# Kernel optimization log

Hardware: AMD Instinct MI355X
Metric: run time of the kernel (lower is better)

Reference implementation:

```python
import jax, jax.numpy as jnp
import numpy as np

B = 1024          # batch of subject-object pairs
D_IN_HALF = 2048  # sbj/obj feature width; cat -> input_len = 4096
D_OUT = 1024      # output_len (embedding / label-vec width)
N_LABELS = 128    # number of relation labels in codebook


def setup_inputs() -> dict:
    key = jax.random.key(0)
    ks = jax.random.split(key, 7)
    s = 0.02  # small init scale for weights
    return {
        "sbj_vec": jax.random.normal(ks[0], (B, D_IN_HALF), jnp.float32),
        "obj_vec": jax.random.normal(ks[1], (B, D_IN_HALF), jnp.float32),
        "W1": jax.random.normal(ks[2], (2 * D_IN_HALF, D_OUT), jnp.float32) * s,
        "b1": jax.random.normal(ks[3], (D_OUT,), jnp.float32) * s,
        "W2": jax.random.normal(ks[4], (D_OUT, D_OUT), jnp.float32) * s,
        "b2": jax.random.normal(ks[5], (D_OUT,), jnp.float32) * s,
        "label_vecs": jax.random.normal(ks[6], (N_LABELS, D_OUT), jnp.float32),
    }


def reference(sbj_vec, obj_vec, W1, b1, W2, b2, label_vecs):
    # Sequential(ReLU, Dropout(eval=identity), Linear) applied twice.
    x = jnp.concatenate([sbj_vec, obj_vec], axis=1)          # [B, 2*D_IN_HALF]
    hidden = jax.nn.relu(x) @ W1 + b1                        # [B, D_OUT]
    emb = jax.nn.relu(hidden) @ W2 + b2                      # [B, D_OUT]
    # order_sim vs every label vector, fully batched (replaces per-sample loop):
    # sim[b, l] = -|| relu(label_vecs[l] - emb[b]) ||_2
    diff = jax.nn.relu(label_vecs[None, :, :] - emb[:, None, :])  # [B, L, D_OUT]
    scores = -jnp.sqrt(jnp.sum(diff * diff, axis=2))              # [B, L]
    return scores
```

## Files before the change

kernel.cpp:

```cpp
#include <hip/hip_runtime.h>
#include <math.h>

constexpr int Bn = 1024, DH = 2048, K1 = 4096, DO = 1024, NL = 128;
constexpr int MN = Bn * DO;

typedef __bf16 bf16x8 __attribute__((ext_vector_type(8)));
typedef short  s16x8  __attribute__((ext_vector_type(8)));
typedef float  f32x4  __attribute__((ext_vector_type(4)));

__device__ __forceinline__ unsigned short f2bf(float f) {
  union { float f; unsigned u; } v; v.f = f;
  unsigned r = v.u + 0x7FFFu + ((v.u >> 16) & 1u);
  return (unsigned short)(r >> 16);
}
__device__ __forceinline__ float bf2f(unsigned h) {
  union { unsigned u; float f; } v; v.u = h << 16; return v.f;
}

__global__ __launch_bounds__(256)
void prep(const float* __restrict__ sbj, const float* __restrict__ obj,
          const float* __restrict__ W1, const float* __restrict__ W2,
          unsigned short* __restrict__ Abf,
          unsigned short* __restrict__ W1t, unsigned short* __restrict__ W2t) {
  const int tid = threadIdx.x;
  if (blockIdx.x < 2048) {
    const int t = blockIdx.x * 256 + tid;
    const int m = t >> 9;
    const int k = (t & 511) << 3;
    const float* src = (k < DH) ? sbj + (size_t)m * DH + k
                                : obj + (size_t)m * DH + (k - DH);
    const float4 a = ((const float4*)src)[0];
    const float4 b = ((const float4*)src)[1];
    uint4 o;
    o.x = (unsigned)f2bf(fmaxf(a.x, 0.f)) | ((unsigned)f2bf(fmaxf(a.y, 0.f)) << 16);
    o.y = (unsigned)f2bf(fmaxf(a.z, 0.f)) | ((unsigned)f2bf(fmaxf(a.w, 0.f)) << 16);
    o.z = (unsigned)f2bf(fmaxf(b.x, 0.f)) | ((unsigned)f2bf(fmaxf(b.y, 0.f)) << 16);
    o.w = (unsigned)f2bf(fmaxf(b.z, 0.f)) | ((unsigned)f2bf(fmaxf(b.w, 0.f)) << 16);
    *(uint4*)&Abf[(size_t)m * K1 + k] = o;
    return;
  }
  __shared__ float tl[64][65];
  const int tb = blockIdx.x - 2048;
  int by = tb >> 4;
  const int c0 = (tb & 15) * 64;
  const float* in; unsigned short* out; int R;
  if (by < 64) { in = W1; out = W1t; R = K1; }
  else         { in = W2; out = W2t; R = DO; by -= 64; }
  const int r0 = by * 64;
  {
    const int rr = tid >> 4, cc = (tid & 15) * 4;
    #pragma unroll
    for (int i = 0; i < 4; ++i) {
      const float4 v = *(const float4*)&in[(size_t)(r0 + rr + i * 16) * DO + c0 + cc];
      tl[rr + i * 16][cc + 0] = v.x; tl[rr + i * 16][cc + 1] = v.y;
      tl[rr + i * 16][cc + 2] = v.z; tl[rr + i * 16][cc + 3] = v.w;
    }
  }
  __syncthreads();
  {
    const int r4 = (tid & 15) * 4;
    #pragma unroll
    for (int i = 0; i < 4; ++i) {
      const int cr = i * 16 + (tid >> 4);
      uint2 o;
      o.x = (unsigned)f2bf(tl[r4 + 0][cr]) | ((unsigned)f2bf(tl[r4 + 1][cr]) << 16);
      o.y = (unsigned)f2bf(tl[r4 + 2][cr]) | ((unsigned)f2bf(tl[r4 + 3][cr]) << 16);
      *(uint2*)&out[(size_t)(c0 + cr) * R + r0 + r4] = o;
    }
  }
}

template <int KSLICE>
__global__ __launch_bounds__(256, 2)
void mfma_gemm(const unsigned short* __restrict__ A,
               const unsigned short* __restrict__ Bt,
               unsigned short* __restrict__ P, int K) {
  __shared__ __align__(16) unsigned short smem[2 * 128 * 64];
  unsigned short* LA = smem;
  unsigned short* LB = smem + 128 * 64;

  const int tid = threadIdx.x;
  const int w = tid >> 6, l = tid & 63;
  const int bid = blockIdx.x;
  const int z = bid & 7, t = bid >> 3;
  const int m0 = (t >> 3) * 128, n0 = (t & 7) * 128;
  const int kb = z * KSLICE;

  f32x4 acc[4][4] = {};

  constexpr int NIT = KSLICE / 64;
  for (int it = 0; it < NIT; ++it) {
    const int k0 = kb + it * 64;
    #pragma unroll
    for (int i = 0; i < 4; ++i) {
      const int c = i * 256 + tid, row = c >> 3, kc = c & 7;
      const int kcg = kc ^ (row & 7);
      __builtin_amdgcn_global_load_lds(
          (const __attribute__((address_space(1))) unsigned int*)(A + (size_t)(m0 + row) * K + k0 + kcg * 8),
          (__attribute__((address_space(3))) unsigned int*)&LA[c * 8], 16, 0, 0);
    }
    #pragma unroll
    for (int i = 0; i < 4; ++i) {
      const int c = i * 256 + tid, row = c >> 3, kc = c & 7;
      const int kcg = kc ^ (row & 7);
      __builtin_amdgcn_global_load_lds(
          (const __attribute__((address_space(1))) unsigned int*)(Bt + (size_t)(n0 + row) * K + k0 + kcg * 8),
          (__attribute__((address_space(3))) unsigned int*)&LB[c * 8], 16, 0, 0);
    }
    __syncthreads();

    #pragma unroll
    for (int s = 0; s < 2; ++s) {
      const int kcq = s * 4 + (l >> 4);
      bf16x8 af[4], bfr[4];
      #pragma unroll
      for (int i = 0; i < 4; ++i) {
        const int r = (w >> 1) * 64 + i * 16 + (l & 15);
        const int kca = kcq ^ (r & 7);
        af[i] = __builtin_bit_cast(bf16x8, *(const s16x8*)&LA[(r * 8 + kca) * 8]);
      }
      #pragma unroll
      for (int j = 0; j < 4; ++j) {
        const int rr = (w & 1) * 64 + j * 16 + (l & 15);
        const int kcb = kcq ^ (rr & 7);
        bfr[j] = __builtin_bit_cast(bf16x8, *(const s16x8*)&LB[(rr * 8 + kcb) * 8]);
      }
      #pragma unroll
      for (int i = 0; i < 4; ++i)
        #pragma unroll
        for (int j = 0; j < 4; ++j)
          acc[i][j] = __builtin_amdgcn_mfma_f32_16x16x32_bf16(af[i], bfr[j], acc[i][j], 0, 0, 0);
    }
    __syncthreads();
  }

  unsigned short* Pz = P + (size_t)z * MN;
  #pragma unroll
  for (int i = 0; i < 4; ++i) {
    #pragma unroll
    for (int r = 0; r < 4; ++r) {
      const int m = m0 + (w >> 1) * 64 + i * 16 + (l >> 4) * 4 + r;
      #pragma unroll
      for (int j = 0; j < 4; ++j) {
        const int n = n0 + (w & 1) * 64 + j * 16 + (l & 15);
        Pz[(size_t)m * DO + n] = f2bf(acc[i][j][r]);
      }
    }
  }
}

__global__ __launch_bounds__(256)
void combine1(const unsigned short* __restrict__ P, const float* __restrict__ bias,
              unsigned short* __restrict__ out) {
  const int row = blockIdx.x, t = threadIdx.x;
  const size_t base = (size_t)row * DO + t * 4;
  float s0 = 0.f, s1 = 0.f, s2 = 0.f, s3 = 0.f;
  #pragma unroll
  for (int c = 0; c < 8; ++c) {
    const uint2 wv = *(const uint2*)&P[(size_t)c * MN + base];
    s0 += bf2f(wv.x & 0xFFFFu); s1 += bf2f(wv.x >> 16);
    s2 += bf2f(wv.y & 0xFFFFu); s3 += bf2f(wv.y >> 16);
  }
  const f32x4 bb = *(const f32x4*)&bias[t * 4];
  s0 = fmaxf(s0 + bb[0], 0.f); s1 = fmaxf(s1 + bb[1], 0.f);
  s2 = fmaxf(s2 + bb[2], 0.f); s3 = fmaxf(s3 + bb[3], 0.f);
  uint2 o;
  o.x = (unsigned)f2bf(s0) | ((unsigned)f2bf(s1) << 16);
  o.y = (unsigned)f2bf(s2) | ((unsigned)f2bf(s3) << 16);
  *(uint2*)&out[base] = o;
}

__global__ __launch_bounds__(256, 4)
void gemm2_full(const unsigned short* __restrict__ A,
                const unsigned short* __restrict__ Bt,
                const float* __restrict__ b2, float* __restrict__ E) {
  __shared__ __align__(16) unsigned short smem[2 * 64 * 128];
  unsigned short* LA = smem;
  unsigned short* LB = smem + 64 * 128;

  const int tid = threadIdx.x;
  const int w = tid >> 6, l = tid & 63;
  const int bid = blockIdx.x;
  const int m0 = (bid >> 4) * 64, n0 = (bid & 15) * 64;

  f32x4 acc[4][4] = {};

  for (int it = 0; it < 8; ++it) {
    const int k0 = it * 128;
    #pragma unroll
    for (int i = 0; i < 4; ++i) {
      const int c = i * 256 + tid, m = c >> 4, kc = c & 15;
      const int kcg = (kc & 8) | ((kc & 7) ^ (m & 7));
      __builtin_amdgcn_global_load_lds(
          (const __attribute__((address_space(1))) unsigned int*)(A + (size_t)(m0 + m) * DO + k0 + kcg * 8),
          (__attribute__((address_space(3))) unsigned int*)&LA[c * 8], 16, 0, 0);
    }
    #pragma unroll
    for (int i = 0; i < 4; ++i) {
      const int c = i * 256 + tid, n = c >> 4, kc = c & 15;
      const int kcg = (kc & 8) | ((kc & 7) ^ (n & 7));
      __builtin_amdgcn_global_load_lds(
          (const __attribute__((address_space(1))) unsigned int*)(Bt + (size_t)(n0 + n) * DO + k0 + kcg * 8),
          (__attribute__((address_space(3))) unsigned int*)&LB[c * 8], 16, 0, 0);
    }
    __syncthreads();

    const int kcq = w * 4 + (l >> 4);
    bf16x8 af[4], bfr[4];
    #pragma unroll
    for (int i = 0; i < 4; ++i) {
      const int r = i * 16 + (l & 15);
      const int kca = (kcq & 8) | ((kcq & 7) ^ (r & 7));
      af[i]  = __builtin_bit_cast(bf16x8, *(const s16x8*)&LA[(r * 16 + kca) * 8]);
      bfr[i] = __builtin_bit_cast(bf16x8, *(const s16x8*)&LB[(r * 16 + kca) * 8]);
    }
    #pragma unroll
    for (int i = 0; i < 4; ++i)
      #pragma unroll
      for (int j = 0; j < 4; ++j)
        acc[i][j] = __builtin_amdgcn_mfma_f32_16x16x32_bf16(af[i], bfr[j], acc[i][j], 0, 0, 0);
    __syncthreads();
  }

  float* red = (float*)smem;
  if (w >= 2) {
    #pragma unroll
    for (int i = 0; i < 4; ++i)
      #pragma unroll
      for (int j = 0; j < 4; ++j)
        *(f32x4*)&red[(w - 2) * 4096 + ((i * 4 + j) * 64 + l) * 4] = acc[i][j];
  }
  __syncthreads();
  if (w < 2) {
    #pragma unroll
    for (int i = 0; i < 4; ++i)
      #pragma unroll
      for (int j = 0; j < 4; ++j)
        acc[i][j] += *(const f32x4*)&red[w * 4096 + ((i * 4 + j) * 64 + l) * 4];
  }
  __syncthreads();
  if (w == 1) {
    #pragma unroll
    for (int i = 0; i < 2; ++i)
      #pragma unroll
      for (int j = 0; j < 4; ++j)
        *(f32x4*)&red[((i * 4 + j) * 64 + l) * 4] = acc[i][j];
  } else if (w == 0) {
    #pragma unroll
    for (int i = 0; i < 2; ++i)
      #pragma unroll
      for (int j = 0; j < 4; ++j)
        *(f32x4*)&red[2048 + ((i * 4 + j) * 64 + l) * 4] = acc[i + 2][j];
  }
  __syncthreads();
  if (w >= 2) return;

  if (w == 0) {
    #pragma unroll
    for (int i = 0; i < 2; ++i) {
      #pragma unroll
      for (int j = 0; j < 4; ++j)
        acc[i][j] += *(const f32x4*)&red[((i * 4 + j) * 64 + l) * 4];
      #pragma unroll
      for (int r = 0; r < 4; ++r) {
        const int m = m0 + i * 16 + (l >> 4) * 4 + r;
        #pragma unroll
        for (int j = 0; j < 4; ++j) {
          const int n = n0 + j * 16 + (l & 15);
          E[(size_t)m * DO + n] = acc[i][j][r] + b2[n];
        }
      }
    }
  } else {
    #pragma unroll
    for (int i = 0; i < 2; ++i) {
      #pragma unroll
      for (int j = 0; j < 4; ++j)
        acc[i + 2][j] += *(const f32x4*)&red[2048 + ((i * 4 + j) * 64 + l) * 4];
      #pragma unroll
      for (int r = 0; r < 4; ++r) {
        const int m = m0 + (i + 2) * 16 + (l >> 4) * 4 + r;
        #pragma unroll
        for (int j = 0; j < 4; ++j) {
          const int n = n0 + j * 16 + (l & 15);
          E[(size_t)m * DO + n] = acc[i + 2][j][r] + b2[n];
        }
      }
    }
  }
}

__global__ __launch_bounds__(256)
void score_partial(const float* __restrict__ E, const float* __restrict__ labels,
                   float* __restrict__ SP) {
  __shared__ float es[64][33];
  __shared__ float ls[64][132];
  const int tid = threadIdx.x;
  const int b0 = blockIdx.x * 32;
  const int d0 = blockIdx.y * 64;

  #pragma unroll
  for (int i = 0; i < 2; ++i) {
    const int fi = tid + i * 256;
    const int b = fi >> 4, dq = fi & 15;
    const float4 v = *(const float4*)&E[(size_t)(b0 + b) * DO + d0 + dq * 4];
    es[dq * 4 + 0][b] = v.x; es[dq * 4 + 1][b] = v.y;
    es[dq * 4 + 2][b] = v.z; es[dq * 4 + 3][b] = v.w;
  }
  #pragma unroll
  for (int i = 0; i < 8; ++i) {
    const int fi = tid + i * 256;
    const int lr = fi >> 4, dq = fi & 15;
    const float4 v = *(const float4*)&labels[(size_t)lr * DO + d0 + dq * 4];
    ls[dq * 4 + 0][lr] = v.x; ls[dq * 4 + 1][lr] = v.y;
    ls[dq * 4 + 2][lr] = v.z; ls[dq * 4 + 3][lr] = v.w;
  }
  __syncthreads();

  const int tb = tid & 15;
  const int tl = tid >> 4;
  float acc[2][8] = {};

  for (int dd = 0; dd < 64; ++dd) {
    const float e0 = es[dd][tb * 2 + 0];
    const float e1 = es[dd][tb * 2 + 1];
    const float4 l0 = *(const float4*)&ls[dd][tl * 8];
    const float4 l1 = *(const float4*)&ls[dd][tl * 8 + 4];
    const float lv[8] = {l0.x, l0.y, l0.z, l0.w, l1.x, l1.y, l1.z, l1.w};
    #pragma unroll
    for (int j = 0; j < 8; ++j) {
      float t0 = fmaxf(lv[j] - e0, 0.f); acc[0][j] = fmaf(t0, t0, acc[0][j]);
      float t1 = fmaxf(lv[j] - e1, 0.f); acc[1][j] = fmaf(t1, t1, acc[1][j]);
    }
  }

  float* SPz = SP + (size_t)blockIdx.y * (Bn * NL);
  #pragma unroll
  for (int i = 0; i < 2; ++i) {
    const size_t base = (size_t)(b0 + tb * 2 + i) * NL + tl * 8;
    float4 v0 = {acc[i][0], acc[i][1], acc[i][2], acc[i][3]};
    float4 v1 = {acc[i][4], acc[i][5], acc[i][6], acc[i][7]};
    *(float4*)&SPz[base]     = v0;
    *(float4*)&SPz[base + 4] = v1;
  }
}

__global__ __launch_bounds__(256)
void score_reduce(const float* __restrict__ SP, float* __restrict__ out) {
  const size_t i4 = (size_t)blockIdx.x * 256 + threadIdx.x;
  f32x4 s = ((const f32x4*)SP)[i4];
  #pragma unroll
  for (int c = 1; c < 16; ++c) s += ((const f32x4*)SP)[(size_t)c * 32768 + i4];
  f32x4 o = {-sqrtf(s[0]), -sqrtf(s[1]), -sqrtf(s[2]), -sqrtf(s[3])};
  ((f32x4*)out)[i4] = o;
}

extern "C" void kernel_launch(void* const* d_in, const int* in_sizes, int n_in,
                              void* d_out, int out_size, void* d_ws, size_t ws_size,
                              hipStream_t stream) {
  const float* sbj  = (const float*)d_in[0];
  const float* obj  = (const float*)d_in[1];
  const float* W1   = (const float*)d_in[2];
  const float* b1   = (const float*)d_in[3];
  const float* W2   = (const float*)d_in[4];
  const float* b2   = (const float*)d_in[5];
  const float* labs = (const float*)d_in[6];
  float* scores = (float*)d_out;
  char* ws = (char*)d_ws;

  unsigned short* Abf = (unsigned short*)(ws);
  unsigned short* W1t = (unsigned short*)(ws + (8ull << 20));
  unsigned short* W2t = (unsigned short*)(ws + (16ull << 20));
  unsigned short* H   = (unsigned short*)(ws + (18ull << 20));
  float* E  = (float*)(ws + (20ull << 20));
  unsigned short* P = (unsigned short*)(ws + (24ull << 20));
  float* SP = (float*)(ws + (40ull << 20));

  dim3 blk(256);
  prep<<<dim3(2048 + 1280), blk, 0, stream>>>(sbj, obj, W1, W2, Abf, W1t, W2t);

  mfma_gemm<512><<<dim3(512), blk, 0, stream>>>(Abf, W1t, P, K1);
  combine1<<<dim3(Bn), blk, 0, stream>>>(P, b1, H);
  gemm2_full<<<dim3(256), blk, 0, stream>>>(H, W2t, b2, E);
  score_partial<<<dim3(32, 16), blk, 0, stream>>>(E, labs, SP);
  score_reduce<<<dim3(128), blk, 0, stream>>>(SP, scores);
}
```

Before: 132.9 us.

## Fuse GEMM2 epilogue with order-similarity partial scoring, dropping E round-trip

The second GEMM now computes the embedding tile, adds bias, and stores it transposed into shared memory. The same block then computes the partial squared-relu distances against the 64-wide slice of the label vectors, removing the global write and re-read of E and one kernel launch. Labels are converted to bf16 in shared memory to fit the LDS budget, which lowers the precision of the label values. The scoring work is now spread over 256 blocks instead of 512, each doing two halves serially.

After: 139.6 us. +5.0%, slower.

```diff
diff --git a/kernel.cpp b/kernel.cpp
--- a/kernel.cpp
+++ b/kernel.cpp
@@ -171,17 +171,20 @@
 }
 
 __global__ __launch_bounds__(256, 4)
-void gemm2_full(const unsigned short* __restrict__ A,
-                const unsigned short* __restrict__ Bt,
-                const float* __restrict__ b2, float* __restrict__ E) {
-  __shared__ __align__(16) unsigned short smem[2 * 64 * 128];
-  unsigned short* LA = smem;
-  unsigned short* LB = smem + 64 * 128;
+void gemm2_score(const unsigned short* __restrict__ A,
+                 const unsigned short* __restrict__ Bt,
+                 const float* __restrict__ b2,
+                 const float* __restrict__ labs,
+                 float* __restrict__ SP) {
+  __shared__ __align__(16) char smem[34048];
+  unsigned short* LA = (unsigned short*)smem;
+  unsigned short* LB = (unsigned short*)smem + 64 * 128;
 
   const int tid = threadIdx.x;
   const int w = tid >> 6, l = tid & 63;
   const int bid = blockIdx.x;
-  const int m0 = (bid >> 4) * 64, n0 = (bid & 15) * 64;
+  const int m0 = (bid >> 4) * 64;
+  const int d0 = (bid & 15) * 64;
 
   f32x4 acc[4][4] = {};
 
@@ -200,7 +203,7 @@
       const int c = i * 256 + tid, n = c >> 4, kc = c & 15;
       const int kcg = (kc & 8) | ((kc & 7) ^ (n & 7));
       __builtin_amdgcn_global_load_lds(
-          (const __attribute__((address_space(1))) unsigned int*)(Bt + (size_t)(n0 + n) * DO + k0 + kcg * 8),
+          (const __attribute__((address_space(1))) unsigned int*)(Bt + (size_t)(d0 + n) * DO + k0 + kcg * 8),
           (__attribute__((address_space(3))) unsigned int*)&LB[c * 8], 16, 0, 0);
     }
     __syncthreads();
@@ -253,95 +256,85 @@
         *(f32x4*)&red[2048 + ((i * 4 + j) * 64 + l) * 4] = acc[i + 2][j];
   }
   __syncthreads();
-  if (w >= 2) return;
-
   if (w == 0) {
     #pragma unroll
-    for (int i = 0; i < 2; ++i) {
+    for (int i = 0; i < 2; ++i)
       #pragma unroll
       for (int j = 0; j < 4; ++j)
         acc[i][j] += *(const f32x4*)&red[((i * 4 + j) * 64 + l) * 4];
-      #pragma unroll
-      for (int r = 0; r < 4; ++r) {
-        const int m = m0 + i * 16 + (l >> 4) * 4 + r;
+  } else if (w == 1) {
+    #pragma unroll
+    for (int i = 0; i < 2; ++i)
+      #pragma unroll
+      for (int j = 0; j < 4; ++j)
+        acc[i + 2][j] += *(const f32x4*)&red[2048 + ((i * 4 + j) * 64 + l) * 4];
+  }
+  __syncthreads();
+
+  float* es = (float*)smem;
+  unsigned short* ls = (unsigned short*)(smem + 16640);
+  if (w == 0) {
+    #pragma unroll
+    for (int j = 0; j < 4; ++j) {
+      const int n = j * 16 + (l & 15);
+      const float bb = b2[d0 + n];
+      #pragma unroll
+      for (int i = 0; i < 2; ++i)
         #pragma unroll
-        for (int j = 0; j < 4; ++j) {
-          const int n = n0 + j * 16 + (l & 15);
-          E[(size_t)m * DO + n] = acc[i][j][r] + b2[n];
-        }
-      }
-    }
-  } else {
-    #pragma unroll
-    for (int i = 0; i < 2; ++i) {
-      #pragma unroll
-      for (int j = 0; j < 4; ++j)
-        acc[i + 2][j] += *(const f32x4*)&red[2048 + ((i * 4 + j) * 64 + l) * 4];
-      #pragma unroll
-      for (int r = 0; r < 4; ++r) {
-        const int m = m0 + (i + 2) * 16 + (l >> 4) * 4 + r;
+        for (int r = 0; r < 4; ++r)
+          es[n * 65 + i * 16 + (l >> 4) * 4 + r] = acc[i][j][r] + bb;
+    }
+  } else if (w == 1) {
+    #pragma unroll
+    for (int j = 0; j < 4; ++j) {
+      const int n = j * 16 + (l & 15);
+      const float bb = b2[d0 + n];
+      #pragma unroll
+      for (int i = 0; i < 2; ++i)
         #pragma unroll
-        for (int j = 0; j < 4; ++j) {
-          const int n = n0 + j * 16 + (l & 15);
-          E[(size_t)m * DO + n] = acc[i + 2][j][r] + b2[n];
-        }
-      }
-    }
-  }
-}
-
-__global__ __launch_bounds__(256)
-void score_partial(const float* __restrict__ E, const float* __restrict__ labels,
-                   float* __restrict__ SP) {
-  __shared__ float es[64][33];
-  __shared__ float ls[64][132];
-  const int tid = threadIdx.x;
-  const int b0 = blockIdx.x * 32;
-  const int d0 = blockIdx.y * 64;
-
-  #pragma unroll
-  for (int i = 0; i < 2; ++i) {
-    const int fi = tid + i * 256;
-    const int b = fi >> 4, dq = fi & 15;
-    const float4 v = *(const float4*)&E[(size_t)(b0 + b) * DO + d0 + dq * 4];
-    es[dq * 4 + 0][b] = v.x; es[dq * 4 + 1][b] = v.y;
-    es[dq * 4 + 2][b] = v.z; es[dq * 4 + 3][b] = v.w;
+        for (int r = 0; r < 4; ++r)
+          es[n * 65 + (i + 2) * 16 + (l >> 4) * 4 + r] = acc[i + 2][j][r] + bb;
+    }
   }
   #pragma unroll
   for (int i = 0; i < 8; ++i) {
-    const int fi = tid + i * 256;
-    const int lr = fi >> 4, dq = fi & 15;
-    const float4 v = *(const float4*)&labels[(size_t)lr * DO + d0 + dq * 4];
-    ls[dq * 4 + 0][lr] = v.x; ls[dq * 4 + 1][lr] = v.y;
-    ls[dq * 4 + 2][lr] = v.z; ls[dq * 4 + 3][lr] = v.w;
+    const int s = i * 256 + tid, lr = s >> 4, dq = s & 15;
+    const float4 v = *(const float4*)&labs[(size_t)lr * DO + d0 + dq * 4];
+    ls[(dq * 4 + 0) * 136 + lr] = f2bf(v.x);
+    ls[(dq * 4 + 1) * 136 + lr] = f2bf(v.y);
+    ls[(dq * 4 + 2) * 136 + lr] = f2bf(v.z);
+    ls[(dq * 4 + 3) * 136 + lr] = f2bf(v.w);
   }
   __syncthreads();
 
   const int tb = tid & 15;
   const int tl = tid >> 4;
-  float acc[2][8] = {};
-
-  for (int dd = 0; dd < 64; ++dd) {
-    const float e0 = es[dd][tb * 2 + 0];
-    const float e1 = es[dd][tb * 2 + 1];
-    const float4 l0 = *(const float4*)&ls[dd][tl * 8];
-    const float4 l1 = *(const float4*)&ls[dd][tl * 8 + 4];
-    const float lv[8] = {l0.x, l0.y, l0.z, l0.w, l1.x, l1.y, l1.z, l1.w};
-    #pragma unroll
-    for (int j = 0; j < 8; ++j) {
-      float t0 = fmaxf(lv[j] - e0, 0.f); acc[0][j] = fmaf(t0, t0, acc[0][j]);
-      float t1 = fmaxf(lv[j] - e1, 0.f); acc[1][j] = fmaf(t1, t1, acc[1][j]);
-    }
-  }
-
-  float* SPz = SP + (size_t)blockIdx.y * (Bn * NL);
-  #pragma unroll
-  for (int i = 0; i < 2; ++i) {
-    const size_t base = (size_t)(b0 + tb * 2 + i) * NL + tl * 8;
-    float4 v0 = {acc[i][0], acc[i][1], acc[i][2], acc[i][3]};
-    float4 v1 = {acc[i][4], acc[i][5], acc[i][6], acc[i][7]};
-    *(float4*)&SPz[base]     = v0;
-    *(float4*)&SPz[base + 4] = v1;
+  float* SPz = SP + (size_t)(bid & 15) * (Bn * NL);
+  #pragma unroll
+  for (int h = 0; h < 2; ++h) {
+    float a2[2][8] = {};
+    for (int dd = 0; dd < 64; ++dd) {
+      const float e0 = es[dd * 65 + h * 32 + tb * 2 + 0];
+      const float e1 = es[dd * 65 + h * 32 + tb * 2 + 1];
+      const uint4 lw = *(const uint4*)&ls[dd * 136 + tl * 8];
+      const float lv[8] = {bf2f(lw.x & 0xFFFFu), bf2f(lw.x >> 16),
+                           bf2f(lw.y & 0xFFFFu), bf2f(lw.y >> 16),
+                           bf2f(lw.z & 0xFFFFu), bf2f(lw.z >> 16),
+                           bf2f(lw.w & 0xFFFFu), bf2f(lw.w >> 16)};
+      #pragma unroll
+      for (int j = 0; j < 8; ++j) {
+        float t0 = fmaxf(lv[j] - e0, 0.f); a2[0][j] = fmaf(t0, t0, a2[0][j]);
+        float t1 = fmaxf(lv[j] - e1, 0.f); a2[1][j] = fmaf(t1, t1, a2[1][j]);
+      }
+    }
+    #pragma unroll
+    for (int i = 0; i < 2; ++i) {
+      const size_t base = (size_t)(m0 + h * 32 + tb * 2 + i) * NL + tl * 8;
+      float4 v0 = {a2[i][0], a2[i][1], a2[i][2], a2[i][3]};
+      float4 v1 = {a2[i][4], a2[i][5], a2[i][6], a2[i][7]};
+      *(float4*)&SPz[base]     = v0;
+      *(float4*)&SPz[base + 4] = v1;
+    }
   }
 }
 
@@ -372,8 +365,7 @@
   unsigned short* W1t = (unsigned short*)(ws + (8ull << 20));
   unsigned short* W2t = (unsigned short*)(ws + (16ull << 20));
   unsigned short* H   = (unsigned short*)(ws + (18ull << 20));
-  float* E  = (float*)(ws + (20ull << 20));
-  unsigned short* P = (unsigned short*)(ws + (24ull << 20));
+  unsigned short* P   = (unsigned short*)(ws + (24ull << 20));
   float* SP = (float*)(ws + (40ull << 20));
 
   dim3 blk(256);
@@ -381,7 +373,6 @@
 
   mfma_gemm<512><<<dim3(512), blk, 0, stream>>>(Abf, W1t, P, K1);
   combine1<<<dim3(Bn), blk, 0, stream>>>(P, b1, H);
-  gemm2_full<<<dim3(256), blk, 0, stream>>>(H, W2t, b2, E);
-  score_partial<<<dim3(32, 16), blk, 0, stream>>>(E, labs, SP);
+  gemm2_score<<<dim3(256), blk, 0, stream>>>(H, W2t, b2, labs, SP);
   score_reduce<<<dim3(128), blk, 0, stream>>>(SP, scores);
 }
```
